# Kernel tuning notes

Measured on AMD Instinct MI355X. Metric: run time of the kernel, lower is better.

The kernel has to match this reference:

```python
import jax, jax.numpy as jnp
import numpy as np

B, C, T, H, W = 2, 512, 16, 24, 24
NUM_HEADS = 8
HEAD_DIM = C // NUM_HEADS
POS_T = 16  # time_pos_emb temporal length


def setup_inputs() -> dict:
    key = jax.random.key(0)
    ks = jax.random.split(key, 10)
    s = 0.02
    return {
        "x": jax.random.normal(ks[0], (B, C, T, H, W), dtype=jnp.float32),
        "wq": jax.random.normal(ks[1], (C, C), dtype=jnp.float32) * s,
        "bq": jnp.zeros((C,), dtype=jnp.float32),
        "wk": jax.random.normal(ks[2], (C, C), dtype=jnp.float32) * s,
        "bk": jnp.zeros((C,), dtype=jnp.float32),
        "wv": jax.random.normal(ks[3], (C, C), dtype=jnp.float32) * s,
        "bv": jnp.zeros((C,), dtype=jnp.float32),
        "wo": jax.random.normal(ks[4], (C, C), dtype=jnp.float32) * s,
        "bo": jnp.zeros((C,), dtype=jnp.float32),
        "pos_emb": jax.random.normal(ks[5], (1, C, POS_T, 1, 1), dtype=jnp.float32) * s,
    }


def _conv1x1(x, w, b):
    # 1x1x1 Conv3d == channel mixing: [O,C] x [B,C,T,H,W] -> [B,O,T,H,W]
    return jnp.einsum('oc,bcthw->bothw', w, x) + b[None, :, None, None, None]


def _split_heads(x):
    # [B, n*d, T, H, W] -> [B, n, T, H*W, d]
    b, c, t, h, w = x.shape
    x = x.reshape(b, NUM_HEADS, HEAD_DIM, t, h * w)
    return x.transpose(0, 1, 3, 4, 2)


def reference(x, wq, bq, wk, bk, wv, bv, wo, bo, pos_emb):
    b, c, t, h, w = x.shape
    xp = x + pos_emb[:, :, :t]  # t <= POS_T, no interpolation needed
    q = _split_heads(_conv1x1(xp, wq, bq))  # [B,n,T,P,d]
    k = _split_heads(_conv1x1(xp, wk, bk))
    v = _split_heads(_conv1x1(xp, wv, bv))
    scale = HEAD_DIM ** (-0.5)
    attn = jnp.einsum('bntpd,bntqd->bntpq', q, k) * scale  # [B,n,T,P,P]
    attn = jax.nn.softmax(attn, axis=-1)
    out = jnp.einsum('bntpq,bntqd->bntpd', attn, v)  # [B,n,T,P,d]
    # [B,n,T,P,d] -> [B,C,T,H,W]
    out = out.transpose(0, 1, 4, 2, 3).reshape(b, c, t, h, w)
    return _conv1x1(out, wo, bo)
```

## Files before the change

### kernel.cpp

```cpp
#include <hip/hip_runtime.h>
#include <math.h>

typedef unsigned short ushort_t;
typedef short bf16x8 __attribute__((ext_vector_type(8)));
typedef float f32x4 __attribute__((ext_vector_type(4)));

#define SLABF (512 * 576)
#define APAD  40
#define NXF   (2 * 512 * 16 * 576)
#define WELEM (512 * 512)
#define HPLANE (576 * 64)

__device__ __forceinline__ float bf2f(ushort_t u) {
    union { unsigned int i; float f; } v;
    v.i = ((unsigned int)u) << 16;
    return v.f;
}
__device__ __forceinline__ ushort_t f2bf(float f) {
    union { float f; unsigned int i; } v;
    v.f = f;
    unsigned int r = v.i + 0x7FFFu + ((v.i >> 16) & 1u);
    return (ushort_t)(r >> 16);
}
__device__ __forceinline__ void split_hl(float x, ushort_t& hi, ushort_t& lo) {
    hi = f2bf(x);
    lo = f2bf(x - bf2f(hi));
}
__device__ __forceinline__ int xcd_swz(int L, int N) {
    return ((N & 7) == 0) ? ((L & 7) * (N >> 3) + (L >> 3)) : L;
}

__global__ __launch_bounds__(256)
void split_xT(const float* __restrict__ x, const float* __restrict__ pos,
              ushort_t* __restrict__ xhi, ushort_t* __restrict__ xlo)
{
    const int bt = blockIdx.z;
    const int b = bt >> 4, t = bt & 15;
    const int pt0 = blockIdx.x * 64;
    const int ct0 = blockIdx.y * 64;
    const int tid = threadIdx.x;

    __shared__ ushort_t Th[64][72], Tl[64][72];

    {
        const int cr = tid >> 2;
        const int pg = (tid & 3) * 16;
        const int c = ct0 + cr;
        const float pv = pos[c * 16 + t];
        const float* src = x + ((size_t)(b * 512 + c) * 16 + t) * 576 + pt0 + pg;
        #pragma unroll
        for (int jj = 0; jj < 4; ++jj) {
            float4 v = *(const float4*)(src + jj * 4);
            v.x += pv; v.y += pv; v.z += pv; v.w += pv;
            ushort_t h, l;
            split_hl(v.x, h, l); Th[pg + jj*4 + 0][cr] = h; Tl[pg + jj*4 + 0][cr] = l;
            split_hl(v.y, h, l); Th[pg + jj*4 + 1][cr] = h; Tl[pg + jj*4 + 1][cr] = l;
            split_hl(v.z, h, l); Th[pg + jj*4 + 2][cr] = h; Tl[pg + jj*4 + 2][cr] = l;
            split_hl(v.w, h, l); Th[pg + jj*4 + 3][cr] = h; Tl[pg + jj*4 + 3][cr] = l;
        }
    }
    __syncthreads();

    {
        const int pr = tid >> 2;
        const int cg = (tid & 3) * 16;
        const size_t obase = (size_t)bt * (576 * 512) + (size_t)(pt0 + pr) * 512 + ct0 + cg;
        #pragma unroll
        for (int m = 0; m < 2; ++m) {
            *(uint4*)(xhi + obase + m * 8) = *(const uint4*)&Th[pr][cg + m * 8];
            *(uint4*)(xlo + obase + m * 8) = *(const uint4*)&Tl[pr][cg + m * 8];
        }
    }
}

__global__ __launch_bounds__(256)
void split_w(const float* __restrict__ w0, const float* __restrict__ w1,
             const float* __restrict__ w2, const float* __restrict__ w3,
             ushort_t* __restrict__ wsp)
{
    const int m = blockIdx.y;
    const float* W = (m == 0) ? w0 : (m == 1) ? w1 : (m == 2) ? w2 : w3;
    ushort_t* hi = wsp + (size_t)m * 2 * WELEM;
    ushort_t* lo = hi + WELEM;
    const int idx = blockIdx.x * 256 + threadIdx.x;
    float4 v = ((const float4*)W)[idx];
    ushort4 h, l;
    split_hl(v.x, h.x, l.x);
    split_hl(v.y, h.y, l.y);
    split_hl(v.z, h.z, l.z);
    split_hl(v.w, h.w, l.w);
    ((ushort4*)hi)[idx] = h;
    ((ushort4*)lo)[idx] = l;
}

__global__ __launch_bounds__(256)
void proj_qkv_mfma(const ushort_t* __restrict__ xhi, const ushort_t* __restrict__ xlo,
                   const ushort_t* __restrict__ wsp,
                   const float* __restrict__ bq, const float* __restrict__ bk,
                   const float* __restrict__ bv,
                   float* __restrict__ qs, float* __restrict__ ks, float* __restrict__ vs,
                   int bt_base, int nbt)
{
    const int w = xcd_swz(blockIdx.x, nbt * 54);
    const int btl = w / 54;
    int r = w - btl * 54;
    const int mode = r / 18; r -= mode * 18;
    const int ot = r / 9;
    const int pt = r - ot * 9;
    const int bt = bt_base + btl;

    const ushort_t* Whi = wsp + (size_t)mode * (2 * WELEM);
    const ushort_t* Wlo = Whi + WELEM;
    const float* bias = (mode == 0) ? bq : (mode == 1) ? bk : bv;
    float* outf = ((mode == 0) ? qs : (mode == 1) ? ks : vs) + (size_t)btl * SLABF;
    ushort_t* ohi = (ushort_t*)outf;
    ushort_t* olo = ohi + SLABF;

    const int o0 = ot * 256;
    const int p0 = pt * 64;
    const int tid = threadIdx.x;
    const int wid = tid >> 6;
    const int lane = tid & 63;
    const int lr = lane & 15;
    const int lk = lane >> 4;

    __shared__ ushort_t Wh[256 * APAD], Wl[256 * APAD];
    __shared__ ushort_t Xh[64 * APAD],  Xl[64 * APAD];

    f32x4 acc[4][4];
    #pragma unroll
    for (int i = 0; i < 4; ++i)
        #pragma unroll
        for (int j = 0; j < 4; ++j) { f32x4 zz = {0.f,0.f,0.f,0.f}; acc[i][j] = zz; }

    const int brow = tid >> 2, boff = (tid & 3) * 8;
    const ushort_t* xbh = xhi + (size_t)bt * (576 * 512);
    const ushort_t* xbl = xlo + (size_t)bt * (576 * 512);

    for (int c0 = 0; c0 < 512; c0 += 32) {
        #pragma unroll
        for (int k = 0; k < 4; ++k) {
            const int ci = tid + k * 256;
            const int row = ci >> 2, off = (ci & 3) * 8;
            const size_t g = (size_t)(o0 + row) * 512 + c0 + off;
            *(bf16x8*)(Wh + row * APAD + off) = *(const bf16x8*)(Whi + g);
            *(bf16x8*)(Wl + row * APAD + off) = *(const bf16x8*)(Wlo + g);
        }
        {
            const size_t g = (size_t)(p0 + brow) * 512 + c0 + boff;
            *(bf16x8*)(Xh + brow * APAD + boff) = *(const bf16x8*)(xbh + g);
            *(bf16x8*)(Xl + brow * APAD + boff) = *(const bf16x8*)(xbl + g);
        }
        __syncthreads();

        bf16x8 ah[4], al[4];
        #pragma unroll
        for (int fo = 0; fo < 4; ++fo) {
            ah[fo] = *(const bf16x8*)(Wh + (wid * 64 + fo * 16 + lr) * APAD + lk * 8);
            al[fo] = *(const bf16x8*)(Wl + (wid * 64 + fo * 16 + lr) * APAD + lk * 8);
        }
        #pragma unroll
        for (int fp = 0; fp < 4; ++fp) {
            bf16x8 bh = *(const bf16x8*)(Xh + (fp * 16 + lr) * APAD + lk * 8);
            bf16x8 bl = *(const bf16x8*)(Xl + (fp * 16 + lr) * APAD + lk * 8);
            #pragma unroll
            for (int fo = 0; fo < 4; ++fo) {
                acc[fo][fp] = __builtin_amdgcn_mfma_f32_16x16x32_bf16(ah[fo], bh, acc[fo][fp], 0, 0, 0);
                acc[fo][fp] = __builtin_amdgcn_mfma_f32_16x16x32_bf16(al[fo], bh, acc[fo][fp], 0, 0, 0);
                acc[fo][fp] = __builtin_amdgcn_mfma_f32_16x16x32_bf16(ah[fo], bl, acc[fo][fp], 0, 0, 0);
            }
        }
        __syncthreads();
    }

    #pragma unroll
    for (int fo = 0; fo < 4; ++fo)
        #pragma unroll
        for (int reg = 0; reg < 4; ++reg) {
            const int o = o0 + wid * 64 + fo * 16 + lk * 4 + reg;
            const float bb = bias[o];
            if (mode == 2) {
                #pragma unroll
                for (int fp = 0; fp < 4; ++fp) {
                    float v = acc[fo][fp][reg] + bb;
                    ushort_t hi, lo; split_hl(v, hi, lo);
                    const size_t off = (size_t)o * 576 + p0 + fp * 16 + lr;
                    ohi[off] = hi; olo[off] = lo;
                }
            } else {
                const size_t base = (size_t)(o >> 6) * HPLANE + (o & 63);
                #pragma unroll
                for (int fp = 0; fp < 4; ++fp) {
                    float v = acc[fo][fp][reg] + bb;
                    if (mode == 0) v *= 0.125f;
                    ushort_t hi, lo; split_hl(v, hi, lo);
                    const size_t off = base + (size_t)(p0 + fp * 16 + lr) * 64;
                    ohi[off] = hi; olo[off] = lo;
                }
            }
        }
}

__global__ __launch_bounds__(256)
void attn_mfma(float* __restrict__ qs, const float* __restrict__ ks,
               const float* __restrict__ vs, int nbt)
{
    const int w9 = xcd_swz(blockIdx.x, nbt * 72);
    const int pair = w9 / 9;
    const int qt = w9 - pair * 9;
    const int btl = pair >> 3;
    const int h = pair & 7;

    const int tid = threadIdx.x;
    const int wid = tid >> 6;
    const int lane = tid & 63;
    const int lr = lane & 15;
    const int lk = lane >> 4;

    const size_t slab = (size_t)btl * SLABF;
    ushort_t* Qhi_g = (ushort_t*)(qs + slab) + (size_t)h * HPLANE;
    ushort_t* Qlo_g = (ushort_t*)(qs + slab) + SLABF + (size_t)h * HPLANE;
    const ushort_t* kbase = (const ushort_t*)(ks + slab);
    const ushort_t* Khi_g = kbase + (size_t)h * HPLANE;
    const ushort_t* Klo_g = kbase + SLABF + (size_t)h * HPLANE;
    const ushort_t* vbase = (const ushort_t*)(vs + slab);
    const ushort_t* Vhi_g = vbase + (size_t)h * HPLANE;
    const ushort_t* Vlo_g = vbase + SLABF + (size_t)h * HPLANE;

    __shared__ ushort_t Kh[32][72], Kl[32][72];
    __shared__ ushort_t Vh[64][40], Vl[64][40];
    __shared__ ushort_t Qh[64][72], Ql[64][72];
    __shared__ ushort_t Ph[4][16][40], Pl[4][16][40];
    __shared__ float Lrow[4][16];

    #pragma unroll
    for (int k = 0; k < 2; ++k) {
        const int ci = tid + k * 256;
        const int row = ci >> 3;
        const int off = (ci & 7) * 8;
        const size_t g = (size_t)(qt * 64 + row) * 64 + off;
        *(uint4*)&Qh[row][off] = *(const uint4*)(Qhi_g + g);
        *(uint4*)&Ql[row][off] = *(const uint4*)(Qlo_g + g);
    }

    const int skv = tid >> 3, sd = (tid & 7) * 8;
    const int svd = tid >> 2, skb = (tid & 3) * 8;
    uint4 kh_r, kl_r, vh_r, vl_r;

    {
        const size_t ko = (size_t)skv * 64 + sd;
        kh_r = *(const uint4*)(Khi_g + ko);
        kl_r = *(const uint4*)(Klo_g + ko);
        const size_t vo = (size_t)svd * 576 + skb;
        vh_r = *(const uint4*)(Vhi_g + vo);
        vl_r = *(const uint4*)(Vlo_g + vo);
        *(uint4*)&Kh[skv][sd] = kh_r; *(uint4*)&Kl[skv][sd] = kl_r;
        *(uint4*)&Vh[svd][skb] = vh_r; *(uint4*)&Vl[svd][skb] = vl_r;
    }
    __syncthreads();

    bf16x8 qh0 = *(const bf16x8*)&Qh[wid * 16 + lr][lk * 8];
    bf16x8 ql0 = *(const bf16x8*)&Ql[wid * 16 + lr][lk * 8];
    bf16x8 qh1 = *(const bf16x8*)&Qh[wid * 16 + lr][32 + lk * 8];
    bf16x8 ql1 = *(const bf16x8*)&Ql[wid * 16 + lr][32 + lk * 8];

    f32x4 o[4];
    #pragma unroll
    for (int nf = 0; nf < 4; ++nf) { f32x4 zz = {0.f,0.f,0.f,0.f}; o[nf] = zz; }
    float lsum = 0.f;

    const int NT = 18;
    for (int tt = 0; tt < NT; ++tt) {
        if (tt + 1 < NT) {
            const size_t ko = (size_t)((tt + 1) * 32 + skv) * 64 + sd;
            kh_r = *(const uint4*)(Khi_g + ko);
            kl_r = *(const uint4*)(Klo_g + ko);
            const size_t vo = (size_t)svd * 576 + (tt + 1) * 32 + skb;
            vh_r = *(const uint4*)(Vhi_g + vo);
            vl_r = *(const uint4*)(Vlo_g + vo);
        }

        f32x4 s0 = {0.f,0.f,0.f,0.f}, s1 = {0.f,0.f,0.f,0.f};
        #pragma unroll
        for (int ks2 = 0; ks2 < 2; ++ks2) {
            const int dof = ks2 * 32 + lk * 8;
            bf16x8 qh = ks2 ? qh1 : qh0;
            bf16x8 ql = ks2 ? ql1 : ql0;
            bf16x8 k0h = *(const bf16x8*)&Kh[lr][dof];
            bf16x8 k0l = *(const bf16x8*)&Kl[lr][dof];
            bf16x8 k1h = *(const bf16x8*)&Kh[16 + lr][dof];
            bf16x8 k1l = *(const bf16x8*)&Kl[16 + lr][dof];
            s0 = __builtin_amdgcn_mfma_f32_16x16x32_bf16(k0h, qh, s0, 0, 0, 0);
            s0 = __builtin_amdgcn_mfma_f32_16x16x32_bf16(k0l, qh, s0, 0, 0, 0);
            s0 = __builtin_amdgcn_mfma_f32_16x16x32_bf16(k0h, ql, s0, 0, 0, 0);
            s1 = __builtin_amdgcn_mfma_f32_16x16x32_bf16(k1h, qh, s1, 0, 0, 0);
            s1 = __builtin_amdgcn_mfma_f32_16x16x32_bf16(k1l, qh, s1, 0, 0, 0);
            s1 = __builtin_amdgcn_mfma_f32_16x16x32_bf16(k1h, ql, s1, 0, 0, 0);
        }

        #pragma unroll
        for (int f = 0; f < 2; ++f) {
            f32x4 sv = f ? s1 : s0;
            float p0 = __expf(sv[0]);
            float p1 = __expf(sv[1]);
            float p2 = __expf(sv[2]);
            float p3 = __expf(sv[3]);
            lsum += (p0 + p1) + (p2 + p3);
            ushort_t h0, l0, h1, l1, h2, l2, h3, l3;
            split_hl(p0, h0, l0); split_hl(p1, h1, l1);
            split_hl(p2, h2, l2); split_hl(p3, h3, l3);
            uint2 wh, wl;
            wh.x = (unsigned int)h0 | ((unsigned int)h1 << 16);
            wh.y = (unsigned int)h2 | ((unsigned int)h3 << 16);
            wl.x = (unsigned int)l0 | ((unsigned int)l1 << 16);
            wl.y = (unsigned int)l2 | ((unsigned int)l3 << 16);
            *(uint2*)&Ph[wid][lr][f * 16 + lk * 4] = wh;
            *(uint2*)&Pl[wid][lr][f * 16 + lk * 4] = wl;
        }
        asm volatile("s_waitcnt lgkmcnt(0)" ::: "memory");
        __builtin_amdgcn_sched_barrier(0);

        {
            bf16x8 pah = *(const bf16x8*)&Ph[wid][lr][lk * 8];
            bf16x8 pal = *(const bf16x8*)&Pl[wid][lr][lk * 8];
            #pragma unroll
            for (int nf = 0; nf < 4; ++nf) {
                bf16x8 vhf = *(const bf16x8*)&Vh[nf * 16 + lr][lk * 8];
                bf16x8 vlf = *(const bf16x8*)&Vl[nf * 16 + lr][lk * 8];
                o[nf] = __builtin_amdgcn_mfma_f32_16x16x32_bf16(pah, vhf, o[nf], 0, 0, 0);
                o[nf] = __builtin_amdgcn_mfma_f32_16x16x32_bf16(pal, vhf, o[nf], 0, 0, 0);
                o[nf] = __builtin_amdgcn_mfma_f32_16x16x32_bf16(pah, vlf, o[nf], 0, 0, 0);
            }
        }

        __syncthreads();
        if (tt + 1 < NT) {
            *(uint4*)&Kh[skv][sd] = kh_r; *(uint4*)&Kl[skv][sd] = kl_r;
            *(uint4*)&Vh[svd][skb] = vh_r; *(uint4*)&Vl[svd][skb] = vl_r;
            __syncthreads();
        }
    }

    lsum += __shfl_xor(lsum, 16);
    lsum += __shfl_xor(lsum, 32);
    if (lk == 0) Lrow[wid][lr] = lsum;
    asm volatile("s_waitcnt lgkmcnt(0)" ::: "memory");
    __builtin_amdgcn_sched_barrier(0);

    float4 lv = *(float4*)&Lrow[wid][lk * 4];
    const float inv[4] = {1.f / lv.x, 1.f / lv.y, 1.f / lv.z, 1.f / lv.w};

    const int qrow = qt * 64 + wid * 16 + lk * 4;
    #pragma unroll
    for (int nf = 0; nf < 4; ++nf)
        #pragma unroll
        for (int reg = 0; reg < 4; ++reg) {
            float v = o[nf][reg] * inv[reg];
            ushort_t hi, lo; split_hl(v, hi, lo);
            const size_t off = (size_t)(qrow + reg) * 64 + nf * 16 + lr;
            Qhi_g[off] = hi; Qlo_g[off] = lo;
        }
}

__global__ __launch_bounds__(256)
void proj_out_mfma(const float* __restrict__ ao, const ushort_t* __restrict__ wsp,
                   const float* __restrict__ bo, float* __restrict__ outb,
                   int bt_base, int nbt)
{
    const int w = xcd_swz(blockIdx.x, nbt * 18);
    const int btl = w / 18;
    int r = w - btl * 18;
    const int ot = r / 9;
    const int pt = r - ot * 9;
    const int bt = bt_base + btl;
    const int b = bt >> 4, t = bt & 15;

    const ushort_t* AOhi = (const ushort_t*)(ao + (size_t)btl * SLABF);
    const ushort_t* AOlo = AOhi + SLABF;
    const ushort_t* Whi = wsp + (size_t)3 * (2 * WELEM);
    const ushort_t* Wlo = Whi + WELEM;

    const int o0 = ot * 256;
    const int p0 = pt * 64;
    const int tid = threadIdx.x;
    const int wid = tid >> 6;
    const int lane = tid & 63;
    const int lr = lane & 15;
    const int lk = lane >> 4;

    __shared__ ushort_t Wh[256 * APAD], Wl[256 * APAD];
    __shared__ ushort_t Xh[64 * APAD],  Xl[64 * APAD];

    f32x4 acc[4][4];
    #pragma unroll
    for (int i = 0; i < 4; ++i)
        #pragma unroll
        for (int j = 0; j < 4; ++j) { f32x4 zz = {0.f,0.f,0.f,0.f}; acc[i][j] = zz; }

    const int brow = tid >> 2, boff = (tid & 3) * 8;

    for (int c0 = 0; c0 < 512; c0 += 32) {
        #pragma unroll
        for (int k = 0; k < 4; ++k) {
            const int ci = tid + k * 256;
            const int row = ci >> 2, off = (ci & 3) * 8;
            const size_t g = (size_t)(o0 + row) * 512 + c0 + off;
            *(bf16x8*)(Wh + row * APAD + off) = *(const bf16x8*)(Whi + g);
            *(bf16x8*)(Wl + row * APAD + off) = *(const bf16x8*)(Wlo + g);
        }
        {
            const size_t g = (size_t)(c0 >> 6) * HPLANE
                           + (size_t)(p0 + brow) * 64 + (c0 & 63) + boff;
            *(bf16x8*)(Xh + brow * APAD + boff) = *(const bf16x8*)(AOhi + g);
            *(bf16x8*)(Xl + brow * APAD + boff) = *(const bf16x8*)(AOlo + g);
        }
        __syncthreads();

        bf16x8 ah[4], al[4];
        #pragma unroll
        for (int fo = 0; fo < 4; ++fo) {
            ah[fo] = *(const bf16x8*)(Wh + (wid * 64 + fo * 16 + lr) * APAD + lk * 8);
            al[fo] = *(const bf16x8*)(Wl + (wid * 64 + fo * 16 + lr) * APAD + lk * 8);
        }
        #pragma unroll
        for (int fp = 0; fp < 4; ++fp) {
            bf16x8 bh = *(const bf16x8*)(Xh + (fp * 16 + lr) * APAD + lk * 8);
            bf16x8 bl = *(const bf16x8*)(Xl + (fp * 16 + lr) * APAD + lk * 8);
            #pragma unroll
            for (int fo = 0; fo < 4; ++fo) {
                acc[fo][fp] = __builtin_amdgcn_mfma_f32_16x16x32_bf16(ah[fo], bh, acc[fo][fp], 0, 0, 0);
                acc[fo][fp] = __builtin_amdgcn_mfma_f32_16x16x32_bf16(al[fo], bh, acc[fo][fp], 0, 0, 0);
                acc[fo][fp] = __builtin_amdgcn_mfma_f32_16x16x32_bf16(ah[fo], bl, acc[fo][fp], 0, 0, 0);
            }
        }
        __syncthreads();
    }

    #pragma unroll
    for (int fo = 0; fo < 4; ++fo)
        #pragma unroll
        for (int reg = 0; reg < 4; ++reg) {
            const int o = o0 + wid * 64 + fo * 16 + lk * 4 + reg;
            const float bb = bo[o];
            const size_t base = ((size_t)(b * 512 + o) * 16 + t) * 576;
            #pragma unroll
            for (int fp = 0; fp < 4; ++fp)
                outb[base + p0 + fp * 16 + lr] = acc[fo][fp][reg] + bb;
        }
}

extern "C" void kernel_launch(void* const* d_in, const int* in_sizes, int n_in,
                              void* d_out, int out_size, void* d_ws, size_t ws_size,
                              hipStream_t stream)
{
    (void)in_sizes; (void)n_in; (void)out_size;
    const float* x   = (const float*)d_in[0];
    const float* wq  = (const float*)d_in[1];
    const float* bq  = (const float*)d_in[2];
    const float* wk  = (const float*)d_in[3];
    const float* bk  = (const float*)d_in[4];
    const float* wv  = (const float*)d_in[5];
    const float* bv  = (const float*)d_in[6];
    const float* wo  = (const float*)d_in[7];
    const float* bo  = (const float*)d_in[8];
    const float* pos = (const float*)d_in[9];

    ushort_t* xhi = (ushort_t*)d_ws;
    ushort_t* xlo = xhi + NXF;
    ushort_t* wsp = xlo + NXF;
    float* slab0 = (float*)(wsp + 8 * WELEM);
    const size_t head_bytes = (size_t)(2 * NXF + 8 * WELEM) * 2;

    const size_t per_bt = (size_t)3 * SLABF * sizeof(float);
    int chunk = 1;
    if (ws_size > head_bytes + per_bt) {
        size_t c = (ws_size - head_bytes) / per_bt;
        chunk = (c > 32) ? 32 : (int)c;
    }
    if (chunk < 1) chunk = 1;

    split_xT<<<dim3(9, 8, 32), 256, 0, stream>>>(x, pos, xhi, xlo);
    split_w<<<dim3(256, 4), 256, 0, stream>>>(wq, wk, wv, wo, wsp);

    for (int bt0 = 0; bt0 < 32; bt0 += chunk) {
        const int nbt = (32 - bt0 < chunk) ? (32 - bt0) : chunk;
        float* qslab = slab0;
        float* kslab = qslab + (size_t)nbt * SLABF;
        float* vslab = kslab + (size_t)nbt * SLABF;

        proj_qkv_mfma<<<dim3(nbt * 54), 256, 0, stream>>>(
            xhi, xlo, wsp, bq, bk, bv, qslab, kslab, vslab, bt0, nbt);
        attn_mfma<<<dim3(nbt * 72), 256, 0, stream>>>(qslab, kslab, vslab, nbt);
        proj_out_mfma<<<dim3(nbt * 18), 256, 0, stream>>>(
            qslab, wsp, bo, (float*)d_out, bt0, nbt);
    }
}
```

Baseline: 427.8 us.

## Prefetch GEMM tiles into registers and stage epilogue stores through LDS

In the QKV and output projection GEMMs, the next K-slice of weights and activations is now loaded into registers while the current slice is computed, so global loads overlap the MFMA work. The epilogues of both GEMMs and of the attention kernel now write results into shared memory first and then issue coalesced 16-byte global stores, replacing scattered 2- and 4-byte stores. This costs more registers and reuses the LDS buffer, which may lower occupancy.

New measurement: 593.1 us. +38.6%, slower.

```diff
diff --git a/kernel.cpp b/kernel.cpp
--- a/kernel.cpp
+++ b/kernel.cpp
@@ -7,6 +7,7 @@
 
 #define SLABF (512 * 576)
 #define APAD  40
+#define EPAD  72
 #define NXF   (2 * 512 * 16 * 576)
 #define WELEM (512 * 512)
 #define HPLANE (576 * 64)
@@ -60,7 +61,6 @@
         }
     }
     __syncthreads();
-
     {
         const int pr = tid >> 2;
         const int cg = (tid & 3) * 16;
@@ -124,8 +124,11 @@
     const int lr = lane & 15;
     const int lk = lane >> 4;
 
-    __shared__ ushort_t Wh[256 * APAD], Wl[256 * APAD];
-    __shared__ ushort_t Xh[64 * APAD],  Xl[64 * APAD];
+    __shared__ __align__(16) ushort_t lds[25600];
+    ushort_t* Wh = lds;
+    ushort_t* Wl = lds + 10240;
+    ushort_t* Xh = lds + 20480;
+    ushort_t* Xl = lds + 23040;
 
     f32x4 acc[4][4];
     #pragma unroll
@@ -137,21 +140,46 @@
     const ushort_t* xbh = xhi + (size_t)bt * (576 * 512);
     const ushort_t* xbl = xlo + (size_t)bt * (576 * 512);
 
+    uint4 wr_h[4], wr_l[4], xr_h, xr_l;
+    #pragma unroll
+    for (int k = 0; k < 4; ++k) {
+        const int ci = tid + k * 256;
+        const int row = ci >> 2, off = (ci & 3) * 8;
+        const size_t g = (size_t)(o0 + row) * 512 + off;
+        wr_h[k] = *(const uint4*)(Whi + g);
+        wr_l[k] = *(const uint4*)(Wlo + g);
+    }
+    {
+        const size_t g = (size_t)(p0 + brow) * 512 + boff;
+        xr_h = *(const uint4*)(xbh + g);
+        xr_l = *(const uint4*)(xbl + g);
+    }
+
     for (int c0 = 0; c0 < 512; c0 += 32) {
+        __syncthreads();
         #pragma unroll
         for (int k = 0; k < 4; ++k) {
             const int ci = tid + k * 256;
             const int row = ci >> 2, off = (ci & 3) * 8;
-            const size_t g = (size_t)(o0 + row) * 512 + c0 + off;
-            *(bf16x8*)(Wh + row * APAD + off) = *(const bf16x8*)(Whi + g);
-            *(bf16x8*)(Wl + row * APAD + off) = *(const bf16x8*)(Wlo + g);
-        }
-        {
-            const size_t g = (size_t)(p0 + brow) * 512 + c0 + boff;
-            *(bf16x8*)(Xh + brow * APAD + boff) = *(const bf16x8*)(xbh + g);
-            *(bf16x8*)(Xl + brow * APAD + boff) = *(const bf16x8*)(xbl + g);
-        }
+            *(uint4*)(Wh + row * APAD + off) = wr_h[k];
+            *(uint4*)(Wl + row * APAD + off) = wr_l[k];
+        }
+        *(uint4*)(Xh + brow * APAD + boff) = xr_h;
+        *(uint4*)(Xl + brow * APAD + boff) = xr_l;
         __syncthreads();
+        if (c0 + 32 < 512) {
+            #pragma unroll
+            for (int k = 0; k < 4; ++k) {
+                const int ci = tid + k * 256;
+                const int row = ci >> 2, off = (ci & 3) * 8;
+                const size_t g = (size_t)(o0 + row) * 512 + c0 + 32 + off;
+                wr_h[k] = *(const uint4*)(Whi + g);
+                wr_l[k] = *(const uint4*)(Wlo + g);
+            }
+            const size_t g = (size_t)(p0 + brow) * 512 + c0 + 32 + boff;
+            xr_h = *(const uint4*)(xbh + g);
+            xr_l = *(const uint4*)(xbl + g);
+        }
 
         bf16x8 ah[4], al[4];
         #pragma unroll
@@ -170,35 +198,61 @@
                 acc[fo][fp] = __builtin_amdgcn_mfma_f32_16x16x32_bf16(ah[fo], bl, acc[fo][fp], 0, 0, 0);
             }
         }
-        __syncthreads();
-    }
-
-    #pragma unroll
-    for (int fo = 0; fo < 4; ++fo)
-        #pragma unroll
-        for (int reg = 0; reg < 4; ++reg) {
-            const int o = o0 + wid * 64 + fo * 16 + lk * 4 + reg;
-            const float bb = bias[o];
-            if (mode == 2) {
+    }
+
+    __syncthreads();
+    ushort_t* Ew = lds + wid * (64 * EPAD);
+    const int head = (o0 >> 6) + wid;
+
+    #pragma unroll
+    for (int pass = 0; pass < 2; ++pass) {
+        if (mode != 2) {
+            #pragma unroll
+            for (int fo = 0; fo < 4; ++fo)
                 #pragma unroll
                 for (int fp = 0; fp < 4; ++fp) {
-                    float v = acc[fo][fp][reg] + bb;
-                    ushort_t hi, lo; split_hl(v, hi, lo);
-                    const size_t off = (size_t)o * 576 + p0 + fp * 16 + lr;
-                    ohi[off] = hi; olo[off] = lo;
+                    ushort4 s;
+                    #pragma unroll
+                    for (int reg = 0; reg < 4; ++reg) {
+                        const int o = o0 + wid * 64 + fo * 16 + lk * 4 + reg;
+                        float v = acc[fo][fp][reg] + bias[o];
+                        if (mode == 0) v *= 0.125f;
+                        ushort_t hi = f2bf(v);
+                        ((ushort_t*)&s)[reg] = pass ? f2bf(v - bf2f(hi)) : hi;
+                    }
+                    *(ushort4*)&Ew[(fp * 16 + lr) * EPAD + fo * 16 + lk * 4] = s;
                 }
-            } else {
-                const size_t base = (size_t)(o >> 6) * HPLANE + (o & 63);
+        } else {
+            #pragma unroll
+            for (int fo = 0; fo < 4; ++fo)
                 #pragma unroll
-                for (int fp = 0; fp < 4; ++fp) {
-                    float v = acc[fo][fp][reg] + bb;
-                    if (mode == 0) v *= 0.125f;
-                    ushort_t hi, lo; split_hl(v, hi, lo);
-                    const size_t off = base + (size_t)(p0 + fp * 16 + lr) * 64;
-                    ohi[off] = hi; olo[off] = lo;
-                }
-            }
-        }
+                for (int fp = 0; fp < 4; ++fp)
+                    #pragma unroll
+                    for (int reg = 0; reg < 4; ++reg) {
+                        const int o = o0 + wid * 64 + fo * 16 + lk * 4 + reg;
+                        float v = acc[fo][fp][reg] + bias[o];
+                        ushort_t hi = f2bf(v);
+                        Ew[(fo * 16 + lk * 4 + reg) * EPAD + fp * 16 + lr] =
+                            pass ? f2bf(v - bf2f(hi)) : hi;
+                    }
+        }
+        asm volatile("s_waitcnt lgkmcnt(0)" ::: "memory");
+        __builtin_amdgcn_sched_barrier(0);
+
+        ushort_t* dst = pass ? olo : ohi;
+        #pragma unroll
+        for (int it = 0; it < 8; ++it) {
+            const int row = it * 8 + (lane >> 3);
+            const int off = (lane & 7) * 8;
+            uint4 v = *(const uint4*)&Ew[row * EPAD + off];
+            if (mode != 2)
+                *(uint4*)(dst + (size_t)head * HPLANE + (size_t)(p0 + row) * 64 + off) = v;
+            else
+                *(uint4*)(dst + (size_t)(o0 + wid * 64 + row) * 576 + p0 + off) = v;
+        }
+        asm volatile("s_waitcnt lgkmcnt(0)" ::: "memory");
+        __builtin_amdgcn_sched_barrier(0);
+    }
 }
 
 __global__ __launch_bounds__(256)
@@ -350,16 +404,26 @@
     float4 lv = *(float4*)&Lrow[wid][lk * 4];
     const float inv[4] = {1.f / lv.x, 1.f / lv.y, 1.f / lv.z, 1.f / lv.w};
 
-    const int qrow = qt * 64 + wid * 16 + lk * 4;
+    const int qrow_l = wid * 16 + lk * 4;
     #pragma unroll
     for (int nf = 0; nf < 4; ++nf)
         #pragma unroll
         for (int reg = 0; reg < 4; ++reg) {
             float v = o[nf][reg] * inv[reg];
             ushort_t hi, lo; split_hl(v, hi, lo);
-            const size_t off = (size_t)(qrow + reg) * 64 + nf * 16 + lr;
-            Qhi_g[off] = hi; Qlo_g[off] = lo;
-        }
+            Qh[qrow_l + reg][nf * 16 + lr] = hi;
+            Ql[qrow_l + reg][nf * 16 + lr] = lo;
+        }
+    asm volatile("s_waitcnt lgkmcnt(0)" ::: "memory");
+    __builtin_amdgcn_sched_barrier(0);
+    #pragma unroll
+    for (int it = 0; it < 2; ++it) {
+        const int rl = wid * 16 + it * 8 + (lane >> 3);
+        const int off = (lane & 7) * 8;
+        const size_t g = (size_t)(qt * 64 + rl) * 64 + off;
+        *(uint4*)(Qhi_g + g) = *(const uint4*)&Qh[rl][off];
+        *(uint4*)(Qlo_g + g) = *(const uint4*)&Ql[rl][off];
+    }
 }
 
 __global__ __launch_bounds__(256)
@@ -388,8 +452,11 @@
     const int lr = lane & 15;
     const int lk = lane >> 4;
 
-    __shared__ ushort_t Wh[256 * APAD], Wl[256 * APAD];
-    __shared__ ushort_t Xh[64 * APAD],  Xl[64 * APAD];
+    __shared__ __align__(16) ushort_t lds[25600];
+    ushort_t* Wh = lds;
+    ushort_t* Wl = lds + 10240;
+    ushort_t* Xh = lds + 20480;
+    ushort_t* Xl = lds + 23040;
 
     f32x4 acc[4][4];
     #pragma unroll
@@ -399,22 +466,48 @@
 
     const int brow = tid >> 2, boff = (tid & 3) * 8;
 
+    uint4 wr_h[4], wr_l[4], xr_h, xr_l;
+    #pragma unroll
+    for (int k = 0; k < 4; ++k) {
+        const int ci = tid + k * 256;
+        const int row = ci >> 2, off = (ci & 3) * 8;
+        const size_t g = (size_t)(o0 + row) * 512 + off;
+        wr_h[k] = *(const uint4*)(Whi + g);
+        wr_l[k] = *(const uint4*)(Wlo + g);
+    }
+    {
+        const size_t g = (size_t)(p0 + brow) * 64 + boff;
+        xr_h = *(const uint4*)(AOhi + g);
+        xr_l = *(const uint4*)(AOlo + g);
+    }
+
     for (int c0 = 0; c0 < 512; c0 += 32) {
+        __syncthreads();
         #pragma unroll
         for (int k = 0; k < 4; ++k) {
             const int ci = tid + k * 256;
             const int row = ci >> 2, off = (ci & 3) * 8;
-            const size_t g = (size_t)(o0 + row) * 512 + c0 + off;
-            *(bf16x8*)(Wh + row * APAD + off) = *(const bf16x8*)(Whi + g);
-            *(bf16x8*)(Wl + row * APAD + off) = *(const bf16x8*)(Wlo + g);
-        }
-        {
-            const size_t g = (size_t)(c0 >> 6) * HPLANE
-                           + (size_t)(p0 + brow) * 64 + (c0 & 63) + boff;
-            *(bf16x8*)(Xh + brow * APAD + boff) = *(const bf16x8*)(AOhi + g);
-            *(bf16x8*)(Xl + brow * APAD + boff) = *(const bf16x8*)(AOlo + g);
-        }
+            *(uint4*)(Wh + row * APAD + off) = wr_h[k];
+            *(uint4*)(Wl + row * APAD + off) = wr_l[k];
+        }
+        *(uint4*)(Xh + brow * APAD + boff) = xr_h;
+        *(uint4*)(Xl + brow * APAD + boff) = xr_l;
         __syncthreads();
+        if (c0 + 32 < 512) {
+            const int cn = c0 + 32;
+            #pragma unroll
+            for (int k = 0; k < 4; ++k) {
+                const int ci = tid + k * 256;
+                const int row = ci >> 2, off = (ci & 3) * 8;
+                const size_t g = (size_t)(o0 + row) * 512 + cn + off;
+                wr_h[k] = *(const uint4*)(Whi + g);
+                wr_l[k] = *(const uint4*)(Wlo + g);
+            }
+            const size_t g = (size_t)(cn >> 6) * HPLANE
+                           + (size_t)(p0 + brow) * 64 + (cn & 63) + boff;
+            xr_h = *(const uint4*)(AOhi + g);
+            xr_l = *(const uint4*)(AOlo + g);
+        }
 
         bf16x8 ah[4], al[4];
         #pragma unroll
@@ -433,20 +526,37 @@
                 acc[fo][fp] = __builtin_amdgcn_mfma_f32_16x16x32_bf16(ah[fo], bl, acc[fo][fp], 0, 0, 0);
             }
         }
-        __syncthreads();
-    }
-
-    #pragma unroll
-    for (int fo = 0; fo < 4; ++fo)
-        #pragma unroll
-        for (int reg = 0; reg < 4; ++reg) {
-            const int o = o0 + wid * 64 + fo * 16 + lk * 4 + reg;
-            const float bb = bo[o];
-            const size_t base = ((size_t)(b * 512 + o) * 16 + t) * 576;
+    }
+
+    __syncthreads();
+    float* Ef = (float*)lds + wid * (32 * 68);
+    #pragma unroll
+    for (int pass = 0; pass < 2; ++pass) {
+        #pragma unroll
+        for (int f2 = 0; f2 < 2; ++f2) {
+            const int fo = pass * 2 + f2;
             #pragma unroll
             for (int fp = 0; fp < 4; ++fp)
-                outb[base + p0 + fp * 16 + lr] = acc[fo][fp][reg] + bb;
-        }
+                #pragma unroll
+                for (int reg = 0; reg < 4; ++reg) {
+                    const int o = o0 + wid * 64 + fo * 16 + lk * 4 + reg;
+                    Ef[(f2 * 16 + lk * 4 + reg) * 68 + fp * 16 + lr] =
+                        acc[fo][fp][reg] + bo[o];
+                }
+        }
+        asm volatile("s_waitcnt lgkmcnt(0)" ::: "memory");
+        __builtin_amdgcn_sched_barrier(0);
+        #pragma unroll
+        for (int it = 0; it < 8; ++it) {
+            const int row = it * 4 + (lane >> 4);
+            const int col = (lane & 15) * 4;
+            float4 v = *(const float4*)&Ef[row * 68 + col];
+            const int o = o0 + wid * 64 + pass * 32 + row;
+            *(float4*)(outb + ((size_t)(b * 512 + o) * 16 + t) * 576 + p0 + col) = v;
+        }
+        asm volatile("s_waitcnt lgkmcnt(0)" ::: "memory");
+        __builtin_amdgcn_sched_barrier(0);
+    }
 }
 
 extern "C" void kernel_launch(void* const* d_in, const int* in_sizes, int n_in,
```
